# Performance work log

Measured on AMD Instinct MI355X. Metric: run time of the kernel, lower is better.

The kernel has to match this reference:

```python
import jax, jax.numpy as jnp
import numpy as np

H = 128          # hidden_channels == num_features for both node types
L = 3            # num_layers
E_TYPES = 3      # (a->a), (a->b), (b->a)
N = 200000       # nodes per type
E = 600000       # edges per edge type
G = 64           # graphs in batch
C = 10           # num_classes
BN_EPS = 1e-5


def setup_inputs() -> dict:
    key = jax.random.key(0)
    ks = jax.random.split(key, 16)
    x_a = jax.random.normal(ks[0], (N, H), dtype=jnp.float32)
    x_b = jax.random.normal(ks[1], (N, H), dtype=jnp.float32)
    ei_aa = jax.random.randint(ks[2], (2, E), 0, N, dtype=jnp.int32)
    ei_ab = jax.random.randint(ks[3], (2, E), 0, N, dtype=jnp.int32)
    ei_ba = jax.random.randint(ks[4], (2, E), 0, N, dtype=jnp.int32)
    batch_a = jnp.sort(jax.random.randint(ks[5], (N,), 0, G, dtype=jnp.int32))
    batch_b = jnp.sort(jax.random.randint(ks[6], (N,), 0, G, dtype=jnp.int32))
    s = 1.0 / np.sqrt(H)
    # GraphConv params per (layer, edge_type): lin_rel (weight+bias), lin_root (no bias)
    Wrel = jax.random.uniform(ks[7], (L, E_TYPES, H, H), jnp.float32, -s, s)
    brel = jax.random.uniform(ks[8], (L, E_TYPES, H), jnp.float32, -s, s)
    Wroot = jax.random.uniform(ks[9], (L, E_TYPES, H, H), jnp.float32, -s, s)
    # BatchNorm affine params per node type (0='a', 1='b')
    bn_gamma = jnp.ones((2, H), jnp.float32)
    bn_beta = jnp.zeros((2, H), jnp.float32)
    lin_W = jax.random.uniform(ks[10], (C, H), jnp.float32, -s, s)
    lin_b = jax.random.uniform(ks[11], (C,), jnp.float32, -s, s)
    return {"x_a": x_a, "x_b": x_b, "Wrel": Wrel, "brel": brel, "Wroot": Wroot,
            "bn_gamma": bn_gamma, "bn_beta": bn_beta, "lin_W": lin_W, "lin_b": lin_b,
            "ei_aa": ei_aa, "ei_ab": ei_ab, "ei_ba": ei_ba,
            "batch_a": batch_a, "batch_b": batch_b}


def _graph_conv(x_src, x_dst, ei, W_rel, b_rel, W_root):
    # PyG GraphConv (aggr='add'): out = lin_rel(sum_{j in N(i)} x_j) + lin_root(x_i)
    agg = jax.ops.segment_sum(x_src[ei[0]], ei[1], num_segments=x_dst.shape[0])
    return agg @ W_rel.T + b_rel + x_dst @ W_root.T


def _bn(x, gamma, beta):
    # BatchNorm in training mode: batch statistics (biased variance)
    mu = x.mean(axis=0)
    var = x.var(axis=0)
    return gamma * (x - mu) * jax.lax.rsqrt(var + BN_EPS) + beta


def reference(x_a, x_b, Wrel, brel, Wroot, bn_gamma, bn_beta, lin_W, lin_b,
              ei_aa, ei_ab, ei_ba, batch_a, batch_b):
    for l in range(L):
        # HeteroConv sums contributions per destination node type
        out_a = (_graph_conv(x_a, x_a, ei_aa, Wrel[l, 0], brel[l, 0], Wroot[l, 0]) +
                 _graph_conv(x_b, x_a, ei_ba, Wrel[l, 2], brel[l, 2], Wroot[l, 2]))
        out_b = _graph_conv(x_a, x_b, ei_ab, Wrel[l, 1], brel[l, 1], Wroot[l, 1])
        x_a = _bn(jax.nn.relu(out_a), bn_gamma[0], bn_beta[0])
        x_b = _bn(jax.nn.relu(out_b), bn_gamma[1], bn_beta[1])
    # global mean pool over concatenated node types
    feats = jnp.concatenate([x_a, x_b], axis=0)
    batch = jnp.concatenate([batch_a, batch_b], axis=0)
    sums = jax.ops.segment_sum(feats, batch, num_segments=G)
    counts = jax.ops.segment_sum(jnp.ones((feats.shape[0],), feats.dtype), batch, num_segments=G)
    pooled = sums / jnp.maximum(counts, 1.0)[:, None]
    return pooled @ lin_W.T + lin_b
```

## Files before the change

### kernel.cpp

```cpp
#include <hip/hip_runtime.h>
#include <hip/hip_bf16.h>

#define HF 128

typedef unsigned int uint32;
typedef unsigned short ushort16;
typedef float f32x4 __attribute__((ext_vector_type(4)));
typedef __bf16 bf16x8 __attribute__((ext_vector_type(8)));

__device__ __forceinline__ float bflo(uint32 u) { return __uint_as_float(u << 16); }
__device__ __forceinline__ float bfhi(uint32 u) { return __uint_as_float(u & 0xffff0000u); }
__device__ __forceinline__ ushort16 f2bf(float f) {
  uint32 u = __float_as_uint(f);
  return (ushort16)((u + 0x7fffu + ((u >> 16) & 1u)) >> 16);
}
__device__ __forceinline__ uint32 pack2(float lo, float hi) {
  return (uint32)f2bf(lo) | ((uint32)f2bf(hi) << 16);
}

__global__ void diag_k(float* __restrict__ out, int n, float val) {
  int i = blockIdx.x * 256 + threadIdx.x;
  if (i < n) out[i] = val;
}

__global__ void init_k(float* __restrict__ ss, float* __restrict__ pool, int Gn) {
  int idx = blockIdx.x * 256 + threadIdx.x;
  if (idx < 512) ss[idx] = (idx < 128 || (idx >= 256 && idx < 384)) ? 1.f : 0.f;
  int p = idx - 512;
  if (p >= 0 && p < Gn * HF) pool[p] = 0.f;
}

__global__ void conv_k(const float* __restrict__ in, uint32* __restrict__ out, int n4) {
  int i = blockIdx.x * 256 + threadIdx.x;
  if (i >= n4) return;
  float4 v = ((const float4*)in)[i];
  uint2 p;
  p.x = pack2(v.x, v.y);
  p.y = pack2(v.z, v.w);
  ((uint2*)out)[i] = p;
}

__global__ void count3_k(const int* __restrict__ eA, int EA, int* __restrict__ rA,
                         const int* __restrict__ eB, int EB, int* __restrict__ rB,
                         const int* __restrict__ eC, int EC, int* __restrict__ rC,
                         int B0, int B1) {
  int b = blockIdx.x;
  const int* ei; int E; int* rp;
  if (b < B0)            { ei = eA; E = EA; rp = rA; }
  else if (b < B0 + B1)  { ei = eB; E = EB; rp = rB; b -= B0; }
  else                   { ei = eC; E = EC; rp = rC; b -= B0 + B1; }
  int e = b * 256 + threadIdx.x;
  if (e < E) atomicAdd(&rp[ei[E + e]], 1);
}

__device__ __forceinline__ void scan1_body(const int* __restrict__ rp, int N,
                                           int* __restrict__ bsum, int b, int t) {
  int i = b * 1024 + t * 4;
  int s = 0;
  if (i + 3 < N) {
    int4 v = *(const int4*)&rp[i];
    s = v.x + v.y + v.z + v.w;
  } else {
    for (int j = 0; j < 4; ++j) if (i + j < N) s += rp[i + j];
  }
  __shared__ int sd[256];
  sd[t] = s;
  __syncthreads();
  for (int o = 128; o > 0; o >>= 1) {
    if (t < o) sd[t] += sd[t + o];
    __syncthreads();
  }
  if (t == 0) bsum[b] = sd[0];
}

__global__ __launch_bounds__(256) void scan1x3_k(
    const int* __restrict__ rA, int NA, int* __restrict__ bA,
    const int* __restrict__ rB, int NB, int* __restrict__ bB,
    const int* __restrict__ rC, int NC, int* __restrict__ bC, int nbA, int nbB) {
  int b = blockIdx.x;
  if (b < nbA)            scan1_body(rA, NA, bA, b, threadIdx.x);
  else if (b < nbA + nbB) scan1_body(rB, NB, bB, b - nbA, threadIdx.x);
  else                    scan1_body(rC, NC, bC, b - nbA - nbB, threadIdx.x);
}

__global__ __launch_bounds__(1024) void scan2x3_k(int* __restrict__ bA, int nbA,
                                                  int* __restrict__ bB, int nbB,
                                                  int* __restrict__ bC, int nbC) {
  int* bsum = (blockIdx.x == 0) ? bA : (blockIdx.x == 1) ? bB : bC;
  int nb    = (blockIdx.x == 0) ? nbA : (blockIdx.x == 1) ? nbB : nbC;
  __shared__ int sd[1024];
  int t = threadIdx.x;
  int v = (t < nb) ? bsum[t] : 0;
  sd[t] = v;
  __syncthreads();
  for (int o = 1; o < 1024; o <<= 1) {
    int x = (t >= o) ? sd[t - o] : 0;
    __syncthreads();
    sd[t] += x;
    __syncthreads();
  }
  if (t < nb) bsum[t] = sd[t] - v;
}

__device__ __forceinline__ void scan3_body(int* __restrict__ rp, int* __restrict__ cur,
                                           const int* __restrict__ bsum, int N,
                                           int b, int t) {
  int i = b * 1024 + t * 4;
  int c[4];
  #pragma unroll
  for (int j = 0; j < 4; ++j) c[j] = (i + j < N) ? rp[i + j] : 0;
  int tsum = c[0] + c[1] + c[2] + c[3];
  __shared__ int sd[256];
  sd[t] = tsum;
  __syncthreads();
  for (int o = 1; o < 256; o <<= 1) {
    int x = (t >= o) ? sd[t - o] : 0;
    __syncthreads();
    sd[t] += x;
    __syncthreads();
  }
  int off = bsum[b] + sd[t] - tsum;
  int p = off;
  #pragma unroll
  for (int j = 0; j < 4; ++j) {
    if (i + j < N) { rp[i + j] = p; cur[i + j] = p; }
    p += c[j];
  }
  if (i < N && N <= i + 4) rp[N] = off + tsum;
}

__global__ __launch_bounds__(256) void scan3x3_k(
    int* __restrict__ rA, int* __restrict__ cA, const int* __restrict__ bA, int NA,
    int* __restrict__ rB, int* __restrict__ cB, const int* __restrict__ bB, int NB,
    int* __restrict__ rC, int* __restrict__ cC, const int* __restrict__ bC, int NC,
    int nbA, int nbB) {
  int b = blockIdx.x;
  if (b < nbA)            scan3_body(rA, cA, bA, NA, b, threadIdx.x);
  else if (b < nbA + nbB) scan3_body(rB, cB, bB, NB, b - nbA, threadIdx.x);
  else                    scan3_body(rC, cC, bC, NC, b - nbA - nbB, threadIdx.x);
}

#define FILL_P 4
__global__ __launch_bounds__(256) void fill3p_k(
    const int* __restrict__ eA, int EA, int* __restrict__ cuA, int* __restrict__ csA,
    const int* __restrict__ eB, int EB, int* __restrict__ cuB, int* __restrict__ csB,
    const int* __restrict__ eC, int EC, int* __restrict__ cuC, int* __restrict__ csC,
    int NA, int NBn, int B0, int B1, int Btot) {
  int pass = blockIdx.x / Btot;
  int b = blockIdx.x % Btot;
  const int* ei; int E; int* cur; int* cs; int N;
  if (b < B0)           { ei = eA; E = EA; cur = cuA; cs = csA; N = NA; }
  else if (b < B0 + B1) { ei = eB; E = EB; cur = cuB; cs = csB; N = NBn; b -= B0; }
  else                  { ei = eC; E = EC; cur = cuC; cs = csC; N = NA; b -= B0 + B1; }
  int e = b * 256 + threadIdx.x;
  if (e >= E) return;
  int dst = ei[E + e];
  int lo = (int)(((long long)pass * N) / FILL_P);
  int hi = (int)(((long long)(pass + 1) * N) / FILL_P);
  if (dst < lo || dst >= hi) return;
  int pos = atomicAdd(&cur[dst], 1);
  cs[pos] = ei[e];
}

__global__ __launch_bounds__(128) void prep2_k(
    const float* __restrict__ Wrel_l, const float* __restrict__ Wroot_l,
    const float* __restrict__ brel_l, const float* __restrict__ ss,
    ushort16* __restrict__ BWa, ushort16* __restrict__ BWb,
    float* __restrict__ uvec, float* __restrict__ stats) {
  __shared__ float red[128];
  int n = blockIdx.x, k = threadIdx.x;
  if (n < 64) {
    float4 z = make_float4(0.f, 0.f, 0.f, 0.f);
    *(float4*)&stats[n * 512 + k * 4] = z;
  }
  float scA = ss[k], shA = ss[128 + k], scB = ss[256 + k], shB = ss[384 + k];
  float w0  = Wrel_l[n * HF + k];
  float w1  = Wrel_l[16384 + n * HF + k];
  float w2  = Wrel_l[32768 + n * HF + k];
  float wr1 = Wroot_l[16384 + n * HF + k];
  float wrc = Wroot_l[n * HF + k] + Wroot_l[32768 + n * HF + k];

  int ksl = k >> 5;
  int lane = (n & 15) + (((k >> 3) & 3) << 4);
  int j = k & 7;
  int nt = n >> 4;
  auto put = [&](ushort16* B, int ksb, float v) {
    B[((size_t)((ksb + ksl) * 8 + nt) * 64 + lane) * 8 + j] = f2bf(v);
  };
  put(BWa, 0, scA * w0);
  put(BWa, 4, scB * w2);
  put(BWa, 8, scA * wrc);
  put(BWb, 0, scA * w1);
  put(BWb, 4, scB * wr1);

  auto reduce = [&](float v) -> float {
    red[k] = v;
    __syncthreads();
    for (int s = 64; s > 0; s >>= 1) {
      if (k < s) red[k] += red[k + s];
      __syncthreads();
    }
    float r = red[0];
    __syncthreads();
    return r;
  };
  float r0 = reduce(shA * w0);
  float r1 = reduce(shB * w2);
  float r2 = reduce(shA * w1);
  float r3 = reduce(shA * wrc);
  float r4 = reduce(shB * wr1);
  if (k == 0) {
    uvec[n]       = r0;
    uvec[128 + n] = r1;
    uvec[256 + n] = r2;
    uvec[384 + n] = brel_l[n] + brel_l[256 + n] + r3;
    uvec[512 + n] = brel_l[128 + n] + r4;
  }
}

template <bool HAS2>
__global__ __launch_bounds__(256) void gg_k(
    const uint32* __restrict__ Xg1, const int* __restrict__ rp1, const int* __restrict__ cs1,
    const uint32* __restrict__ Xg2, const int* __restrict__ rp2, const int* __restrict__ cs2,
    const uint32* Xr,
    const bf16x8* __restrict__ BW,
    const float* __restrict__ u1, const float* __restrict__ u2,
    const float* __restrict__ bias,
    uint32* out,
    float* __restrict__ statS, float* __restrict__ statQ,
    int nRows) {
  constexpr int KS_G = HAS2 ? 8 : 4;
  __shared__ uint32 lds[4][1088];
  int tid = threadIdx.x, wid = tid >> 6, l = tid & 63;
  int R0 = blockIdx.x * 64 + wid * 16;
  uint32* L = &lds[wid][0];
  int row = l & 15, khi = l >> 4;
  int myRow = R0 + row;

  float lo[16], hi[16];
  auto addv = [&](int base, uint4 v) {
    hi[base + 0] += __uint_as_float(v.x); lo[base + 0] += __uint_as_float(v.x << 16);
    hi[base + 1] += __uint_as_float(v.y); lo[base + 1] += __uint_as_float(v.y << 16);
    hi[base + 2] += __uint_as_float(v.z); lo[base + 2] += __uint_as_float(v.z << 16);
    hi[base + 3] += __uint_as_float(v.w); lo[base + 3] += __uint_as_float(v.w << 16);
  };
  auto gather_reg = [&](const uint32* __restrict__ Xg, const int* __restrict__ rp,
                        const int* __restrict__ cs) {
    #pragma unroll
    for (int i = 0; i < 16; ++i) { lo[i] = 0.f; hi[i] = 0.f; }
    if (myRow < nRows) {
      int e0 = rp[myRow], e1 = rp[myRow + 1];
      int e = e0;
      for (; e + 2 <= e1; e += 2) {
        int s0 = cs[e], s1 = cs[e + 1];
        const uint32* p0 = &Xg[(size_t)s0 * 64 + khi * 4];
        const uint32* p1 = &Xg[(size_t)s1 * 64 + khi * 4];
        uint4 v0 = *(const uint4*)&p0[0];
        uint4 v1 = *(const uint4*)&p0[16];
        uint4 v2 = *(const uint4*)&p0[32];
        uint4 v3 = *(const uint4*)&p0[48];
        uint4 w0 = *(const uint4*)&p1[0];
        uint4 w1 = *(const uint4*)&p1[16];
        uint4 w2 = *(const uint4*)&p1[32];
        uint4 w3 = *(const uint4*)&p1[48];
        addv(0, v0); addv(4, v1); addv(8, v2); addv(12, v3);
        addv(0, w0); addv(4, w1); addv(8, w2); addv(12, w3);
      }
      if (e < e1) {
        const uint32* p0 = &Xg[(size_t)cs[e] * 64 + khi * 4];
        addv(0,  *(const uint4*)&p0[0]);
        addv(4,  *(const uint4*)&p0[16]);
        addv(8,  *(const uint4*)&p0[32]);
        addv(12, *(const uint4*)&p0[48]);
      }
    }
  };
  auto to_frag = [&](int ks) -> bf16x8 {
    bf16x8 a;
    #pragma unroll
    for (int j = 0; j < 4; ++j) {
      a[2 * j]     = (__bf16)lo[ks * 4 + j];
      a[2 * j + 1] = (__bf16)hi[ks * 4 + j];
    }
    return a;
  };

  f32x4 acc[8] = {};
  const bf16x8* Bl = BW + l;

  gather_reg(Xg1, rp1, cs1);
  {
    bf16x8 af[4];
    #pragma unroll
    for (int ks = 0; ks < 4; ++ks) af[ks] = to_frag(ks);
    #pragma unroll
    for (int ks = 0; ks < 4; ++ks) {
      #pragma unroll
      for (int nt = 0; nt < 8; ++nt) {
        bf16x8 b = Bl[(size_t)(ks * 8 + nt) * 64];
        acc[nt] = __builtin_amdgcn_mfma_f32_16x16x32_bf16(af[ks], b, acc[nt], 0, 0, 0);
      }
    }
  }
  if constexpr (HAS2) {
    gather_reg(Xg2, rp2, cs2);
    bf16x8 af[4];
    #pragma unroll
    for (int ks = 0; ks < 4; ++ks) af[ks] = to_frag(ks);
    #pragma unroll
    for (int ks = 0; ks < 4; ++ks) {
      #pragma unroll
      for (int nt = 0; nt < 8; ++nt) {
        bf16x8 b = Bl[(size_t)((4 + ks) * 8 + nt) * 64];
        acc[nt] = __builtin_amdgcn_mfma_f32_16x16x32_bf16(af[ks], b, acc[nt], 0, 0, 0);
      }
    }
  }
  #pragma unroll
  for (int ks = 0; ks < 4; ++ks) {
    bf16x8 a{};
    if (myRow < nRows) a = *(const bf16x8*)&Xr[(size_t)myRow * 64 + (ks * 4 + khi) * 4];
    #pragma unroll
    for (int nt = 0; nt < 8; ++nt) {
      bf16x8 b = Bl[(size_t)((KS_G + ks) * 8 + nt) * 64];
      acc[nt] = __builtin_amdgcn_mfma_f32_16x16x32_bf16(a, b, acc[nt], 0, 0, 0);
    }
  }

  int rl0 = khi * 4;
  float deg1v[4], deg2v[4];
  #pragma unroll
  for (int j = 0; j < 4; ++j) {
    int r = R0 + rl0 + j;
    deg1v[j] = (r < nRows) ? (float)(rp1[r + 1] - rp1[r]) : 0.f;
    if constexpr (HAS2) deg2v[j] = (r < nRows) ? (float)(rp2[r + 1] - rp2[r]) : 0.f;
    else deg2v[j] = 0.f;
  }
  ushort16* P = (ushort16*)L;
  int c0 = l & 15;
  float ps[8], pq[8];
  #pragma unroll
  for (int nt = 0; nt < 8; ++nt) {
    int col = nt * 16 + c0;
    float bc = bias[col];
    float u1c = u1[col];
    float u2c = HAS2 ? u2[col] : 0.f;
    float s = 0.f, q = 0.f;
    #pragma unroll
    for (int j = 0; j < 4; ++j) {
      float v = acc[nt][j] + bc + deg1v[j] * u1c;
      if constexpr (HAS2) v += deg2v[j] * u2c;
      v = fmaxf(v, 0.f);
      if (R0 + rl0 + j < nRows) { s += v; q += v * v; }
      P[(rl0 + j) * 136 + col] = f2bf(v);
    }
    ps[nt] = s; pq[nt] = q;
  }

  #pragma unroll
  for (int rr = 0; rr < 4; ++rr) {
    int rloc = rr * 4 + khi;
    int grow = R0 + rloc;
    if (grow < nRows) {
      uint4 v = *(const uint4*)&P[rloc * 136 + c0 * 8];
      *(uint4*)&out[(size_t)grow * 64 + c0 * 4] = v;
    }
  }

  #pragma unroll
  for (int nt = 0; nt < 8; ++nt) {
    ps[nt] += __shfl_xor(ps[nt], 16); ps[nt] += __shfl_xor(ps[nt], 32);
    pq[nt] += __shfl_xor(pq[nt], 16); pq[nt] += __shfl_xor(pq[nt], 32);
  }
  if (l < 16) {
    float* S = statS + (size_t)(blockIdx.x & 63) * 128;
    float* Q = statQ + (size_t)(blockIdx.x & 63) * 128;
    #pragma unroll
    for (int nt = 0; nt < 8; ++nt) {
      unsafeAtomicAdd(&S[nt * 16 + l], ps[nt]);
      unsafeAtomicAdd(&Q[nt * 16 + l], pq[nt]);
    }
  }
}

__global__ void bn_fin_k(const float* __restrict__ stats, const float* __restrict__ gamma,
                         const float* __restrict__ beta, float* __restrict__ ss,
                         float nA, float nB) {
  int t = threadIdx.x;
  if (t >= 256) return;
  int type = t >> 7, f = t & 127;
  const float* S = stats + (size_t)type * 16384;
  const float* Q = S + 8192;
  float s = 0.f, q = 0.f;
  for (int st = 0; st < 64; ++st) { s += S[st * 128 + f]; q += Q[st * 128 + f]; }
  float nN = type ? nB : nA;
  float mean = s / nN;
  float var = q / nN - mean * mean;
  float rstd = rsqrtf(var + 1e-5f);
  float sc = gamma[type * HF + f] * rstd;
  float sh = beta[type * HF + f] - mean * sc;
  ss[type * 256 + f] = sc;
  ss[type * 256 + 128 + f] = sh;
}

__global__ __launch_bounds__(256) void pool_k(const uint32* __restrict__ x,
                                              const int* __restrict__ batch,
                                              const float* __restrict__ scale,
                                              const float* __restrict__ shift,
                                              float* __restrict__ pool, int nN) {
  int f2 = threadIdx.x & 31;
  int sub = threadIdx.x >> 5;
  int start = blockIdx.x * 1024;
  int end = min(start + 1024, nN);
  float4 sc = *(const float4*)&scale[f2 * 4];
  float4 sh = *(const float4*)&shift[f2 * 4];
  float a0 = 0.f, a1 = 0.f, a2 = 0.f, a3 = 0.f, cnt = 0.f;
  int cur = -1;
  for (int n = start + sub; n < end; n += 8) {
    int g = batch[n];
    if (g != cur) {
      if (cur >= 0) {
        float* bp = &pool[(size_t)cur * HF + f2 * 4];
        unsafeAtomicAdd(bp + 0, sc.x * a0 + cnt * sh.x);
        unsafeAtomicAdd(bp + 1, sc.y * a1 + cnt * sh.y);
        unsafeAtomicAdd(bp + 2, sc.z * a2 + cnt * sh.z);
        unsafeAtomicAdd(bp + 3, sc.w * a3 + cnt * sh.w);
      }
      a0 = a1 = a2 = a3 = 0.f; cnt = 0.f; cur = g;
    }
    uint2 v = *(const uint2*)&x[(size_t)n * 64 + f2 * 2];
    a0 += bflo(v.x); a1 += bfhi(v.x); a2 += bflo(v.y); a3 += bfhi(v.y);
    cnt += 1.f;
  }
  if (cur >= 0) {
    float* bp = &pool[(size_t)cur * HF + f2 * 4];
    unsafeAtomicAdd(bp + 0, sc.x * a0 + cnt * sh.x);
    unsafeAtomicAdd(bp + 1, sc.y * a1 + cnt * sh.y);
    unsafeAtomicAdd(bp + 2, sc.z * a2 + cnt * sh.z);
    unsafeAtomicAdd(bp + 3, sc.w * a3 + cnt * sh.w);
  }
}

__device__ inline int lowerb(const int* a, int n, int v) {
  int lo = 0, hi = n;
  while (lo < hi) { int m = (lo + hi) >> 1; if (a[m] < v) lo = m + 1; else hi = m; }
  return lo;
}

__global__ void counts_k(const int* __restrict__ ba, int nA, const int* __restrict__ bb, int nB,
                         float* __restrict__ counts, int Gn) {
  for (int g = threadIdx.x; g < Gn; g += blockDim.x) {
    int c = (lowerb(ba, nA, g + 1) - lowerb(ba, nA, g)) +
            (lowerb(bb, nB, g + 1) - lowerb(bb, nB, g));
    counts[g] = fmaxf((float)c, 1.f);
  }
}

__global__ void final_k(const float* __restrict__ pool, const float* __restrict__ counts,
                        const float* __restrict__ linW, const float* __restrict__ linb,
                        float* __restrict__ out, int Cn) {
  int g = blockIdx.x;
  int lane = threadIdx.x;
  float inv = 1.f / counts[g];
  float p0 = pool[(size_t)g * HF + lane] * inv;
  float p1 = pool[(size_t)g * HF + 64 + lane] * inv;
  for (int c = 0; c < Cn; ++c) {
    float t = p0 * linW[c * HF + lane] + p1 * linW[c * HF + 64 + lane];
    for (int off = 32; off > 0; off >>= 1) t += __shfl_down(t, off);
    if (lane == 0) out[g * Cn + c] = t + linb[c];
  }
}

extern "C" void kernel_launch(void* const* d_in, const int* in_sizes, int n_in,
                              void* d_out, int out_size, void* d_ws, size_t ws_size,
                              hipStream_t stream) {
  const float* x_a   = (const float*)d_in[0];
  const float* x_b   = (const float*)d_in[1];
  const float* Wrel  = (const float*)d_in[2];
  const float* brel  = (const float*)d_in[3];
  const float* Wroot = (const float*)d_in[4];
  const float* bn_g  = (const float*)d_in[5];
  const float* bn_b  = (const float*)d_in[6];
  const float* lin_W = (const float*)d_in[7];
  const float* lin_b = (const float*)d_in[8];
  const int* ei_aa   = (const int*)d_in[9];
  const int* ei_ab   = (const int*)d_in[10];
  const int* ei_ba   = (const int*)d_in[11];
  const int* batch_a = (const int*)d_in[12];
  const int* batch_b = (const int*)d_in[13];

  int Na  = in_sizes[0] / HF;
  int Nb  = in_sizes[1] / HF;
  int Eaa = in_sizes[9] / 2;
  int Eab = in_sizes[10] / 2;
  int Eba = in_sizes[11] / 2;
  int Cn  = in_sizes[7] / HF;
  int Gn  = out_size / Cn;

  size_t NHa = (size_t)Na * HF, NHb = (size_t)Nb * HF;
  char* base = (char*)d_ws;
  auto alignup = [](size_t x) { return (x + 255) & ~(size_t)255; };
  size_t off = 0;
  size_t oXA0 = off; off = alignup(off + NHa * 2);
  size_t oXA1 = off; off = alignup(off + NHa * 2);
  size_t oXB  = off; off = alignup(off + NHb * 2);
  size_t oRP  = off; off = alignup(off + ((size_t)(Na + 1) + (Nb + 1) + (Na + 1)) * 4);
  size_t oCUR = off; off = alignup(off + ((size_t)Na + Nb + Na) * 4);
  size_t oCS  = off; off = alignup(off + ((size_t)Eaa + Eab + Eba + 16) * 4);
  size_t oBWA = off; off = alignup(off + (size_t)12 * 8 * 64 * 16);
  size_t oBWB = off; off = alignup(off + (size_t)8 * 8 * 64 * 16);
  size_t oUV  = off; off = alignup(off + 5 * 128 * 4);
  size_t oSS  = off; off = alignup(off + 512 * 4);
  size_t oST  = off; off = alignup(off + 32768 * 4);
  size_t oBS  = off; off = alignup(off + 3072 * 4);
  size_t oPOOL= off; off = alignup(off + (size_t)Gn * HF * 4);
  size_t oCNT = off; off = alignup(off + (size_t)Gn * 4);
  size_t need = off;

  if (ws_size < need) {
    diag_k<<<(out_size + 255) / 256, 256, 0, stream>>>(
        (float*)d_out, out_size, (float)((double)ws_size / 1048576.0));
    return;
  }

  uint32* XA0 = (uint32*)(base + oXA0);
  uint32* XA1 = (uint32*)(base + oXA1);
  uint32* XB  = (uint32*)(base + oXB);
  int* rp_aa = (int*)(base + oRP);
  int* rp_ab = rp_aa + (Na + 1);
  int* rp_ba = rp_ab + (Nb + 1);
  int* cur_aa = (int*)(base + oCUR);
  int* cur_ab = cur_aa + Na;
  int* cur_ba = cur_ab + Nb;
  int* cs_aa = (int*)(base + oCS);
  int* cs_ab = cs_aa + Eaa;
  int* cs_ba = cs_ab + Eab;
  ushort16* BWa = (ushort16*)(base + oBWA);
  ushort16* BWb = (ushort16*)(base + oBWB);
  float* uvec  = (float*)(base + oUV);
  float* ss    = (float*)(base + oSS);
  float* stats = (float*)(base + oST);
  int* bsum    = (int*)(base + oBS);
  float* pool  = (float*)(base + oPOOL);
  float* counts= (float*)(base + oCNT);

  float* ss_a = ss;
  float* ss_b = ss + 256;
  float* uaa = uvec, *uba = uvec + 128, *uab = uvec + 256;
  float* bias_a = uvec + 384, *bias_b = uvec + 512;
  float* SA = stats, *QA = stats + 8192, *SB = stats + 16384, *QB = stats + 24576;

  init_k<<<(512 + Gn * HF + 255) / 256, 256, 0, stream>>>(ss, pool, Gn);
  conv_k<<<((int)(NHa / 4) + 255) / 256, 256, 0, stream>>>(x_a, XA0, (int)(NHa / 4));
  conv_k<<<((int)(NHb / 4) + 255) / 256, 256, 0, stream>>>(x_b, XB, (int)(NHb / 4));

  hipMemsetAsync(rp_aa, 0, ((size_t)(Na + 1) + (Nb + 1) + (Na + 1)) * 4, stream);
  int B0 = (Eaa + 255) / 256, B1 = (Eab + 255) / 256, B2 = (Eba + 255) / 256;
  count3_k<<<B0 + B1 + B2, 256, 0, stream>>>(ei_aa, Eaa, rp_aa, ei_ab, Eab, rp_ab,
                                             ei_ba, Eba, rp_ba, B0, B1);

  int nb_a = (Na + 1023) / 1024;
  int nb_b = (Nb + 1023) / 1024;
  scan1x3_k<<<nb_a + nb_b + nb_a, 256, 0, stream>>>(
      rp_aa, Na, bsum, rp_ab, Nb, bsum + 1024, rp_ba, Na, bsum + 2048, nb_a, nb_b);
  scan2x3_k<<<3, 1024, 0, stream>>>(bsum, nb_a, bsum + 1024, nb_b, bsum + 2048, nb_a);
  scan3x3_k<<<nb_a + nb_b + nb_a, 256, 0, stream>>>(
      rp_aa, cur_aa, bsum, Na, rp_ab, cur_ab, bsum + 1024, Nb,
      rp_ba, cur_ba, bsum + 2048, Na, nb_a, nb_b);

  int Btot = B0 + B1 + B2;
  fill3p_k<<<FILL_P * Btot, 256, 0, stream>>>(ei_aa, Eaa, cur_aa, cs_aa,
                                              ei_ab, Eab, cur_ab, cs_ab,
                                              ei_ba, Eba, cur_ba, cs_ba,
                                              Na, Nb, B0, B1, Btot);

  uint32* xa_cur = XA0;
  uint32* xa_nxt = XA1;
  for (int l = 0; l < 3; ++l) {
    const float* Wrel_l  = Wrel  + (size_t)l * 3 * 16384;
    const float* Wroot_l = Wroot + (size_t)l * 3 * 16384;
    const float* brel_l  = brel  + (size_t)l * 3 * HF;

    prep2_k<<<128, 128, 0, stream>>>(Wrel_l, Wroot_l, brel_l, ss, BWa, BWb, uvec, stats);

    gg_k<true><<<(Na + 63) / 64, 256, 0, stream>>>(
        xa_cur, rp_aa, cs_aa, XB, rp_ba, cs_ba, xa_cur,
        (const bf16x8*)BWa, uaa, uba, bias_a, xa_nxt, SA, QA, Na);
    gg_k<false><<<(Nb + 63) / 64, 256, 0, stream>>>(
        xa_cur, rp_ab, cs_ab, nullptr, nullptr, nullptr, XB,
        (const bf16x8*)BWb, uab, nullptr, bias_b, XB, SB, QB, Nb);

    bn_fin_k<<<1, 256, 0, stream>>>(stats, bn_g, bn_b, ss, (float)Na, (float)Nb);

    uint32* t = xa_cur; xa_cur = xa_nxt; xa_nxt = t;
  }

  pool_k<<<(Na + 1023) / 1024, 256, 0, stream>>>(xa_cur, batch_a, ss_a, ss_a + 128, pool, Na);
  pool_k<<<(Nb + 1023) / 1024, 256, 0, stream>>>(XB, batch_b, ss_b, ss_b + 128, pool, Nb);
  counts_k<<<1, 256, 0, stream>>>(batch_a, Na, batch_b, Nb, counts, Gn);
  final_k<<<Gn, 64, 0, stream>>>(pool, counts, lin_W, lin_b, (float*)d_out, Cn);
}
```

Before: 1.045 ms.

## Pad CSR rows to multiples of four with zero-row sentinel to unroll gathers

Each destination row's neighbour list in the CSR is padded up to a multiple of four, and the padding slots point at an extra all-zero feature row appended to every feature buffer. The gather loop can then always take four neighbours per iteration with no remainder handling. True degrees are kept in a separate array for the degree-dependent terms, and out-of-range rows read the zero row instead of branching. The cost is up to three extra gathers per row, extra CSR memory, and additional init and zeroing kernels.

```diff
diff --git a/kernel.cpp b/kernel.cpp
--- a/kernel.cpp
+++ b/kernel.cpp
@@ -28,6 +28,14 @@
   if (idx < 512) ss[idx] = (idx < 128 || (idx >= 256 && idx < 384)) ? 1.f : 0.f;
   int p = idx - 512;
   if (p >= 0 && p < Gn * HF) pool[p] = 0.f;
+}
+
+__global__ void zrow_k(uint32* __restrict__ a0, uint32* __restrict__ a1,
+                       uint32* __restrict__ b, size_t offA, size_t offB) {
+  int t = threadIdx.x;
+  if (t < 64) a0[offA + t] = 0;
+  else if (t < 128) a1[offA + (t - 64)] = 0;
+  else if (t < 192) b[offB + (t - 128)] = 0;
 }
 
 __global__ void conv_k(const float* __restrict__ in, uint32* __restrict__ out, int n4) {
@@ -38,6 +46,16 @@
   p.x = pack2(v.x, v.y);
   p.y = pack2(v.z, v.w);
   ((uint2*)out)[i] = p;
+}
+
+__global__ void initcs_k(int* __restrict__ cs, size_t c0, size_t c1, size_t c2,
+                         int vA, int vB) {
+  size_t i = ((size_t)blockIdx.x * 256 + threadIdx.x) * 4;
+  size_t tot = c0 + c1 + c2;
+  if (i >= tot) return;
+  int v = (i < c0 + c1) ? vA : vB;
+  int4 w = make_int4(v, v, v, v);
+  *(int4*)&cs[i] = w;
 }
 
 __global__ void count3_k(const int* __restrict__ eA, int EA, int* __restrict__ rA,
@@ -53,15 +71,17 @@
   if (e < E) atomicAdd(&rp[ei[E + e]], 1);
 }
 
+__device__ __forceinline__ int pad4(int c) { return (c + 3) & ~3; }
+
 __device__ __forceinline__ void scan1_body(const int* __restrict__ rp, int N,
                                            int* __restrict__ bsum, int b, int t) {
   int i = b * 1024 + t * 4;
   int s = 0;
   if (i + 3 < N) {
     int4 v = *(const int4*)&rp[i];
-    s = v.x + v.y + v.z + v.w;
+    s = pad4(v.x) + pad4(v.y) + pad4(v.z) + pad4(v.w);
   } else {
-    for (int j = 0; j < 4; ++j) if (i + j < N) s += rp[i + j];
+    for (int j = 0; j < 4; ++j) if (i + j < N) s += pad4(rp[i + j]);
   }
   __shared__ int sd[256];
   sd[t] = s;
@@ -103,13 +123,14 @@
 }
 
 __device__ __forceinline__ void scan3_body(int* __restrict__ rp, int* __restrict__ cur,
+                                           int* __restrict__ deg,
                                            const int* __restrict__ bsum, int N,
                                            int b, int t) {
   int i = b * 1024 + t * 4;
   int c[4];
   #pragma unroll
   for (int j = 0; j < 4; ++j) c[j] = (i + j < N) ? rp[i + j] : 0;
-  int tsum = c[0] + c[1] + c[2] + c[3];
+  int tsum = pad4(c[0]) + pad4(c[1]) + pad4(c[2]) + pad4(c[3]);
   __shared__ int sd[256];
   sd[t] = tsum;
   __syncthreads();
@@ -123,21 +144,24 @@
   int p = off;
   #pragma unroll
   for (int j = 0; j < 4; ++j) {
-    if (i + j < N) { rp[i + j] = p; cur[i + j] = p; }
-    p += c[j];
+    if (i + j < N) { rp[i + j] = p; cur[i + j] = p; deg[i + j] = c[j]; }
+    p += pad4(c[j]);
   }
   if (i < N && N <= i + 4) rp[N] = off + tsum;
 }
 
 __global__ __launch_bounds__(256) void scan3x3_k(
-    int* __restrict__ rA, int* __restrict__ cA, const int* __restrict__ bA, int NA,
-    int* __restrict__ rB, int* __restrict__ cB, const int* __restrict__ bB, int NB,
-    int* __restrict__ rC, int* __restrict__ cC, const int* __restrict__ bC, int NC,
+    int* __restrict__ rA, int* __restrict__ cA, int* __restrict__ dA,
+    const int* __restrict__ bA, int NA,
+    int* __restrict__ rB, int* __restrict__ cB, int* __restrict__ dB,
+    const int* __restrict__ bB, int NB,
+    int* __restrict__ rC, int* __restrict__ cC, int* __restrict__ dC,
+    const int* __restrict__ bC, int NC,
     int nbA, int nbB) {
   int b = blockIdx.x;
-  if (b < nbA)            scan3_body(rA, cA, bA, NA, b, threadIdx.x);
-  else if (b < nbA + nbB) scan3_body(rB, cB, bB, NB, b - nbA, threadIdx.x);
-  else                    scan3_body(rC, cC, bC, NC, b - nbA - nbB, threadIdx.x);
+  if (b < nbA)            scan3_body(rA, cA, dA, bA, NA, b, threadIdx.x);
+  else if (b < nbA + nbB) scan3_body(rB, cB, dB, bB, NB, b - nbA, threadIdx.x);
+  else                    scan3_body(rC, cC, dC, bC, NC, b - nbA - nbB, threadIdx.x);
 }
 
 #define FILL_P 4
@@ -221,7 +245,9 @@
 template <bool HAS2>
 __global__ __launch_bounds__(256) void gg_k(
     const uint32* __restrict__ Xg1, const int* __restrict__ rp1, const int* __restrict__ cs1,
+    const int* __restrict__ deg1,
     const uint32* __restrict__ Xg2, const int* __restrict__ rp2, const int* __restrict__ cs2,
+    const int* __restrict__ deg2,
     const uint32* Xr,
     const bf16x8* __restrict__ BW,
     const float* __restrict__ u1, const float* __restrict__ u2,
@@ -236,6 +262,8 @@
   uint32* L = &lds[wid][0];
   int row = l & 15, khi = l >> 4;
   int myRow = R0 + row;
+  bool okRow = myRow < nRows;
+  int rowIdx = okRow ? myRow : nRows;
 
   float lo[16], hi[16];
   auto addv = [&](int base, uint4 v) {
@@ -248,30 +276,34 @@
                         const int* __restrict__ cs) {
     #pragma unroll
     for (int i = 0; i < 16; ++i) { lo[i] = 0.f; hi[i] = 0.f; }
-    if (myRow < nRows) {
+    if (okRow) {
       int e0 = rp[myRow], e1 = rp[myRow + 1];
-      int e = e0;
-      for (; e + 2 <= e1; e += 2) {
-        int s0 = cs[e], s1 = cs[e + 1];
-        const uint32* p0 = &Xg[(size_t)s0 * 64 + khi * 4];
-        const uint32* p1 = &Xg[(size_t)s1 * 64 + khi * 4];
-        uint4 v0 = *(const uint4*)&p0[0];
-        uint4 v1 = *(const uint4*)&p0[16];
-        uint4 v2 = *(const uint4*)&p0[32];
-        uint4 v3 = *(const uint4*)&p0[48];
-        uint4 w0 = *(const uint4*)&p1[0];
-        uint4 w1 = *(const uint4*)&p1[16];
-        uint4 w2 = *(const uint4*)&p1[32];
-        uint4 w3 = *(const uint4*)&p1[48];
-        addv(0, v0); addv(4, v1); addv(8, v2); addv(12, v3);
-        addv(0, w0); addv(4, w1); addv(8, w2); addv(12, w3);
-      }
-      if (e < e1) {
-        const uint32* p0 = &Xg[(size_t)cs[e] * 64 + khi * 4];
-        addv(0,  *(const uint4*)&p0[0]);
-        addv(4,  *(const uint4*)&p0[16]);
-        addv(8,  *(const uint4*)&p0[32]);
-        addv(12, *(const uint4*)&p0[48]);
+      for (int e = e0; e < e1; e += 4) {
+        int i0 = cs[e], i1 = cs[e + 1], i2 = cs[e + 2], i3 = cs[e + 3];
+        const uint32* p0 = &Xg[(size_t)i0 * 64 + khi * 4];
+        const uint32* p1 = &Xg[(size_t)i1 * 64 + khi * 4];
+        const uint32* p2 = &Xg[(size_t)i2 * 64 + khi * 4];
+        const uint32* p3 = &Xg[(size_t)i3 * 64 + khi * 4];
+        uint4 a0 = *(const uint4*)&p0[0];
+        uint4 a1 = *(const uint4*)&p0[16];
+        uint4 a2 = *(const uint4*)&p0[32];
+        uint4 a3 = *(const uint4*)&p0[48];
+        uint4 b0 = *(const uint4*)&p1[0];
+        uint4 b1 = *(const uint4*)&p1[16];
+        uint4 b2 = *(const uint4*)&p1[32];
+        uint4 b3 = *(const uint4*)&p1[48];
+        uint4 c0 = *(const uint4*)&p2[0];
+        uint4 c1 = *(const uint4*)&p2[16];
+        uint4 c2 = *(const uint4*)&p2[32];
+        uint4 c3 = *(const uint4*)&p2[48];
+        uint4 d0 = *(const uint4*)&p3[0];
+        uint4 d1 = *(const uint4*)&p3[16];
+        uint4 d2 = *(const uint4*)&p3[32];
+        uint4 d3 = *(const uint4*)&p3[48];
+        addv(0, a0); addv(4, a1); addv(8, a2); addv(12, a3);
+        addv(0, b0); addv(4, b1); addv(8, b2); addv(12, b3);
+        addv(0, c0); addv(4, c1); addv(8, c2); addv(12, c3);
+        addv(0, d0); addv(4, d1); addv(8, d2); addv(12, d3);
       }
     }
   };
@@ -318,8 +350,7 @@
   }
   #pragma unroll
   for (int ks = 0; ks < 4; ++ks) {
-    bf16x8 a{};
-    if (myRow < nRows) a = *(const bf16x8*)&Xr[(size_t)myRow * 64 + (ks * 4 + khi) * 4];
+    bf16x8 a = *(const bf16x8*)&Xr[(size_t)rowIdx * 64 + (ks * 4 + khi) * 4];
     #pragma unroll
     for (int nt = 0; nt < 8; ++nt) {
       bf16x8 b = Bl[(size_t)((KS_G + ks) * 8 + nt) * 64];
@@ -332,8 +363,8 @@
   #pragma unroll
   for (int j = 0; j < 4; ++j) {
     int r = R0 + rl0 + j;
-    deg1v[j] = (r < nRows) ? (float)(rp1[r + 1] - rp1[r]) : 0.f;
-    if constexpr (HAS2) deg2v[j] = (r < nRows) ? (float)(rp2[r + 1] - rp2[r]) : 0.f;
+    deg1v[j] = (r < nRows) ? (float)deg1[r] : 0.f;
+    if constexpr (HAS2) deg2v[j] = (r < nRows) ? (float)deg2[r] : 0.f;
     else deg2v[j] = 0.f;
   }
   ushort16* P = (ushort16*)L;
@@ -498,15 +529,20 @@
   int Gn  = out_size / Cn;
 
   size_t NHa = (size_t)Na * HF, NHb = (size_t)Nb * HF;
+  size_t capA = ((size_t)Eaa + 3 * (size_t)Na + 15) & ~(size_t)15;
+  size_t capB = ((size_t)Eab + 3 * (size_t)Nb + 15) & ~(size_t)15;
+  size_t capC = ((size_t)Eba + 3 * (size_t)Na + 15) & ~(size_t)15;
+
   char* base = (char*)d_ws;
   auto alignup = [](size_t x) { return (x + 255) & ~(size_t)255; };
   size_t off = 0;
-  size_t oXA0 = off; off = alignup(off + NHa * 2);
-  size_t oXA1 = off; off = alignup(off + NHa * 2);
-  size_t oXB  = off; off = alignup(off + NHb * 2);
+  size_t oXA0 = off; off = alignup(off + (NHa + HF) * 2);
+  size_t oXA1 = off; off = alignup(off + (NHa + HF) * 2);
+  size_t oXB  = off; off = alignup(off + (NHb + HF) * 2);
   size_t oRP  = off; off = alignup(off + ((size_t)(Na + 1) + (Nb + 1) + (Na + 1)) * 4);
   size_t oCUR = off; off = alignup(off + ((size_t)Na + Nb + Na) * 4);
-  size_t oCS  = off; off = alignup(off + ((size_t)Eaa + Eab + Eba + 16) * 4);
+  size_t oDEG = off; off = alignup(off + ((size_t)Na + Nb + Na) * 4);
+  size_t oCS  = off; off = alignup(off + (capA + capB + capC) * 4);
   size_t oBWA = off; off = alignup(off + (size_t)12 * 8 * 64 * 16);
   size_t oBWB = off; off = alignup(off + (size_t)8 * 8 * 64 * 16);
   size_t oUV  = off; off = alignup(off + 5 * 128 * 4);
@@ -532,9 +568,12 @@
   int* cur_aa = (int*)(base + oCUR);
   int* cur_ab = cur_aa + Na;
   int* cur_ba = cur_ab + Nb;
+  int* deg_aa = (int*)(base + oDEG);
+  int* deg_ab = deg_aa + Na;
+  int* deg_ba = deg_ab + Nb;
   int* cs_aa = (int*)(base + oCS);
-  int* cs_ab = cs_aa + Eaa;
-  int* cs_ba = cs_ab + Eab;
+  int* cs_ab = cs_aa + capA;
+  int* cs_ba = cs_ab + capB;
   ushort16* BWa = (ushort16*)(base + oBWA);
   ushort16* BWb = (ushort16*)(base + oBWB);
   float* uvec  = (float*)(base + oUV);
@@ -553,6 +592,7 @@
   init_k<<<(512 + Gn * HF + 255) / 256, 256, 0, stream>>>(ss, pool, Gn);
   conv_k<<<((int)(NHa / 4) + 255) / 256, 256, 0, stream>>>(x_a, XA0, (int)(NHa / 4));
   conv_k<<<((int)(NHb / 4) + 255) / 256, 256, 0, stream>>>(x_b, XB, (int)(NHb / 4));
+  zrow_k<<<1, 256, 0, stream>>>(XA0, XA1, XB, NHa / 2, NHb / 2);
 
   hipMemsetAsync(rp_aa, 0, ((size_t)(Na + 1) + (Nb + 1) + (Na + 1)) * 4, stream);
   int B0 = (Eaa + 255) / 256, B1 = (Eab + 255) / 256, B2 = (Eba + 255) / 256;
@@ -565,8 +605,13 @@
       rp_aa, Na, bsum, rp_ab, Nb, bsum + 1024, rp_ba, Na, bsum + 2048, nb_a, nb_b);
   scan2x3_k<<<3, 1024, 0, stream>>>(bsum, nb_a, bsum + 1024, nb_b, bsum + 2048, nb_a);
   scan3x3_k<<<nb_a + nb_b + nb_a, 256, 0, stream>>>(
-      rp_aa, cur_aa, bsum, Na, rp_ab, cur_ab, bsum + 1024, Nb,
-      rp_ba, cur_ba, bsum + 2048, Na, nb_a, nb_b);
+      rp_aa, cur_aa, deg_aa, bsum, Na,
+      rp_ab, cur_ab, deg_ab, bsum + 1024, Nb,
+      rp_ba, cur_ba, deg_ba, bsum + 2048, Na, nb_a, nb_b);
+
+  size_t capTot = capA + capB + capC;
+  initcs_k<<<(int)((capTot / 4 + 255) / 256), 256, 0, stream>>>(
+      cs_aa, capA, capB, capC, Na, Nb);
 
   int Btot = B0 + B1 + B2;
   fill3p_k<<<FILL_P * Btot, 256, 0, stream>>>(ei_aa, Eaa, cur_aa, cs_aa,
@@ -584,10 +629,10 @@
     prep2_k<<<128, 128, 0, stream>>>(Wrel_l, Wroot_l, brel_l, ss, BWa, BWb, uvec, stats);
 
     gg_k<true><<<(Na + 63) / 64, 256, 0, stream>>>(
-        xa_cur, rp_aa, cs_aa, XB, rp_ba, cs_ba, xa_cur,
+        xa_cur, rp_aa, cs_aa, deg_aa, XB, rp_ba, cs_ba, deg_ba, xa_cur,
         (const bf16x8*)BWa, uaa, uba, bias_a, xa_nxt, SA, QA, Na);
     gg_k<false><<<(Nb + 63) / 64, 256, 0, stream>>>(
-        xa_cur, rp_ab, cs_ab, nullptr, nullptr, nullptr, XB,
+        xa_cur, rp_ab, cs_ab, deg_ab, nullptr, nullptr, nullptr, nullptr, XB,
         (const bf16x8*)BWb, uab, nullptr, bias_b, XB, SB, QB, Nb);
 
     bn_fin_k<<<1, 256, 0, stream>>>(stats, bn_g, bn_b, ss, (float)Na, (float)Nb);
```

Result: slower. 1.088 ms (+4.1%).
